# Kernel tuning notes

Hardware: AMD Instinct MI355X
Metric: run time of the kernel (lower is better)

Reference implementation:

```python
import jax, jax.numpy as jnp
import numpy as np
from jax import lax

L, H, NUM_CONVS, KSIZE = 8192, 128, 4, 7
EPS = 1e-5


def _pos_encoding(length, dim, dtype):
    pos = jnp.arange(length, dtype=jnp.float32)[:, None]
    i = jnp.arange(dim, dtype=jnp.float32)[None, :]
    angle = pos / jnp.power(10000.0, (2.0 * jnp.floor(i / 2.0)) / dim)
    pe = jnp.where((jnp.arange(dim) % 2 == 0)[None, :], jnp.sin(angle), jnp.cos(angle))
    return pe.astype(dtype)


def _layer_norm(x):
    mu = jnp.mean(x, axis=-1, keepdims=True)
    var = jnp.mean(jnp.square(x - mu), axis=-1, keepdims=True)
    return (x - mu) * lax.rsqrt(var + EPS)


def _conv1d_same(x, w, b):
    # x: [L, H]; w: [H_out, H_in, K]; b: [H_out]. SAME padding over sequence.
    lhs = x.T[None]  # [1, H, L]
    out = lax.conv_general_dilated(lhs, w, window_strides=(1,), padding='SAME',
                                   dimension_numbers=('NCH', 'OIH', 'NCH'))
    return (out[0] + b[:, None]).T  # [L, H]


def setup_inputs() -> dict:
    key = jax.random.key(0)
    ks = jax.random.split(key, 12)
    s = 0.02
    return {
        'x': jax.random.normal(ks[0], (L, H), jnp.float32),
        'conv_w': jax.random.normal(ks[1], (NUM_CONVS, H, H, KSIZE), jnp.float32) * s,
        'conv_b': jax.random.normal(ks[2], (NUM_CONVS, H), jnp.float32) * s,
        'Wq': jax.random.normal(ks[3], (H, H), jnp.float32) * s,
        'bq': jax.random.normal(ks[4], (H,), jnp.float32) * s,
        'Wk': jax.random.normal(ks[5], (H, H), jnp.float32) * s,
        'bk': jax.random.normal(ks[6], (H,), jnp.float32) * s,
        'Wv': jax.random.normal(ks[7], (H, H), jnp.float32) * s,
        'bv': jax.random.normal(ks[8], (H,), jnp.float32) * s,
        'Wff': jax.random.normal(ks[9], (H, H), jnp.float32) * s,
        'bff': jax.random.normal(ks[10], (H,), jnp.float32) * s,
    }


def reference(x, conv_w, conv_b, Wq, bq, Wk, bk, Wv, bv, Wff, bff):
    h = x + _pos_encoding(x.shape[0], x.shape[1], x.dtype)
    # conv stack: LN -> conv -> residual, repeated num_convs times
    for i in range(NUM_CONVS):
        residual = h
        h = _conv1d_same(_layer_norm(h), conv_w[i], conv_b[i]) + residual
    # self-attention (single-head as written in the source)
    residual = h
    n = _layer_norm(h)
    q = n @ Wq.T + bq
    k = n @ Wk.T + bk
    v = n @ Wv.T + bv
    scale = 1.0 / jnp.sqrt(jnp.asarray(H, h.dtype))
    attn = jax.nn.softmax((q @ k.T) * scale, axis=-1)  # [L, L]
    h = attn @ v + residual
    # feed-forward
    residual = h
    h = jax.nn.relu(_layer_norm(h) @ Wff.T + bff) + residual
    return h
```

## Files before the change

kernel.cpp:

```cpp
#include <hip/hip_runtime.h>

#define LL 8192
#define HH 128

typedef __attribute__((ext_vector_type(8))) short short8v;
typedef __attribute__((ext_vector_type(4))) short short4v;
typedef __attribute__((ext_vector_type(4))) float f32x4;

__device__ inline short f2bf(float f) {
    union { float f; unsigned u; } x; x.f = f;
    unsigned r = (x.u + 0x7fffu + ((x.u >> 16) & 1u)) >> 16;
    return (short)r;
}
__device__ inline float bf2f(short s) {
    union { unsigned u; float f; } x; x.u = ((unsigned)(unsigned short)s) << 16;
    return x.f;
}

__device__ inline short* sAp(short* base, int row, int col) {
    int byte = (row << 8) + (col << 1);
    byte ^= (row & 7) << 4;
    return (short*)((char*)base + byte);
}

__device__ inline short8v ln_pack8(const float* rowF, int l15) {
    const float4 a = *(const float4*)&rowF[l15 * 8];
    const float4 b = *(const float4*)&rowF[l15 * 8 + 4];
    float s  = (a.x + a.y) + (a.z + a.w) + (b.x + b.y) + (b.z + b.w);
    float s2 = a.x * a.x + a.y * a.y + a.z * a.z + a.w * a.w
             + b.x * b.x + b.y * b.y + b.z * b.z + b.w * b.w;
#pragma unroll
    for (int off = 1; off <= 8; off <<= 1) {
        s  += __shfl_xor(s,  off, 64);
        s2 += __shfl_xor(s2, off, 64);
    }
    float mu = s * (1.f / 128.f);
    float var = s2 * (1.f / 128.f) - mu * mu;
    float rstd = rsqrtf(var + 1e-5f);
    short8v r;
    r[0] = f2bf((a.x - mu) * rstd);
    r[1] = f2bf((a.y - mu) * rstd);
    r[2] = f2bf((a.z - mu) * rstd);
    r[3] = f2bf((a.w - mu) * rstd);
    r[4] = f2bf((b.x - mu) * rstd);
    r[5] = f2bf((b.y - mu) * rstd);
    r[6] = f2bf((b.z - mu) * rstd);
    r[7] = f2bf((b.w - mu) * rstd);
    return r;
}

__global__ __launch_bounds__(256) void repack_all(const float* __restrict__ x,
                                                  const float* __restrict__ w,
                                                  const float* __restrict__ Wq,
                                                  const float* __restrict__ Wk,
                                                  const float* __restrict__ Wv,
                                                  const float* __restrict__ bq,
                                                  const float* __restrict__ bk,
                                                  const float* __restrict__ bv,
                                                  const float* __restrict__ Wff,
                                                  short* __restrict__ wkb,
                                                  short* __restrict__ wqkvb,
                                                  float* __restrict__ b3,
                                                  short* __restrict__ wffb,
                                                  float* __restrict__ h0) {
    const float qs = 0.08838834764831845f;
    int idx = blockIdx.x * 256 + threadIdx.x;
    if (idx < 458752) {
        int k = idx % 7;
        int t = idx / 7;
        int i = t % HH; t /= HH;
        int o = t % HH;
        int lay = t / HH;
        wkb[((lay * 7 + k) * HH + o) * HH + i] = f2bf(w[idx]);
    } else {
        int j = idx - 458752;
        if (j < 49152) {
            int t = j >> 14, r = j & 16383;
            float v = (t == 0) ? Wq[r] * qs : (t == 1) ? Wk[r] : Wv[r];
            wqkvb[j] = f2bf(v);
        } else if (j < 49536) {
            int jj = j - 49152;
            b3[jj] = (jj < 128) ? bq[jj] * qs : (jj < 256) ? bk[jj - 128] : bv[jj - 256];
        } else if (j < 65920) {
            int jj = j - 49536;
            wffb[jj] = f2bf(Wff[jj]);
        } else {
            int p = j - 65920;
            if (p < 262144) {
                int g = p >> 5, c4 = (p & 31) << 2;
                float4 val = *(const float4*)&x[g * HH + c4];
                float fg = (float)g;
#pragma unroll
                for (int h = 0; h < 2; h++) {
                    int i0 = c4 + h * 2;
                    float e = (float)i0 / 128.f;
                    float ang = fg / powf(10000.f, e);
                    ((float*)&val)[h * 2]     += sinf(ang);
                    ((float*)&val)[h * 2 + 1] += cosf(ang);
                }
                *(float4*)&h0[g * HH + c4] = val;
            }
        }
    }
}

__global__ __launch_bounds__(256, 4) void conv_layer_kernel(const float* __restrict__ hin,
                                                            const short* __restrict__ wkb,
                                                            const float* __restrict__ conv_b,
                                                            float* __restrict__ hout,
                                                            int lay) {
    __shared__ float sF[22][132];
    __shared__ short sA[22 * 128];
    int tid = threadIdx.x;
    int w = tid >> 6, lane = tid & 63;
    int l15 = lane & 15, quad = lane >> 4;
    int m0 = (blockIdx.x >> 1) * 16;
    int c0w = (blockIdx.x & 1) * 64 + w * 16;

    for (int idx = tid; idx < 22 * 32; idx += 256) {
        int r = idx >> 5, c4 = (idx & 31) << 2;
        int g = m0 - 3 + r;
        float4 val = make_float4(0.f, 0.f, 0.f, 0.f);
        if (g >= 0 && g < LL) val = *(const float4*)&hin[g * HH + c4];
        *(float4*)&sF[r][c4] = val;
    }
    __syncthreads();
#pragma unroll
    for (int rr = 0; rr < 2; rr++) {
        int row = rr * 16 + w * 4 + quad;
        if (row < 22)
            *(short8v*)sAp(sA, row, l15 * 8) = ln_pack8(&sF[row][0], l15);
    }
    __syncthreads();
    f32x4 accA = (f32x4)(0.f), accB = (f32x4)(0.f);
    const short* wl = wkb + lay * 7 * HH * HH;
    for (int k = 0; k < 7; k++) {
        const short* b0 = wl + (k * HH + c0w + l15) * HH;
#pragma unroll
        for (int ks = 0; ks < 4; ks++) {
            short8v bf = *(const short8v*)&b0[ks * 32 + quad * 8];
            short8v af = *(const short8v*)sAp(sA, l15 + k, ks * 32 + quad * 8);
            if (ks & 1) accB = __builtin_amdgcn_mfma_f32_16x16x32_bf16(af, bf, accB, 0, 0, 0);
            else        accA = __builtin_amdgcn_mfma_f32_16x16x32_bf16(af, bf, accA, 0, 0, 0);
        }
    }
    float bb = conv_b[lay * HH + c0w + l15];
#pragma unroll
    for (int r = 0; r < 4; r++) {
        int row = quad * 4 + r;
        hout[(m0 + row) * HH + c0w + l15] =
            sF[3 + row][c0w + l15] + accA[r] + accB[r] + bb;
    }
}

__global__ __launch_bounds__(256, 4) void qkv_kernel(const float* __restrict__ h4,
                                                     const short* __restrict__ wqkvb,
                                                     const float* __restrict__ b3,
                                                     short* __restrict__ qb,
                                                     short* __restrict__ kb,
                                                     short* __restrict__ vt) {
    __shared__ float sF[16][132];
    __shared__ short sA[16 * 128];
    __shared__ short sT[4][32][17];
    int tid = threadIdx.x;
    int w = tid >> 6, lane = tid & 63;
    int l15 = lane & 15, quad = lane >> 4;
    int m0 = blockIdx.x * 16;
    int t = blockIdx.y;

    for (int idx = tid; idx < 16 * 32; idx += 256) {
        int r = idx >> 5, c4 = (idx & 31) << 2;
        *(float4*)&sF[r][c4] = *(const float4*)&h4[(m0 + r) * HH + c4];
    }
    __syncthreads();
    {
        int row = w * 4 + quad;
        *(short8v*)sAp(sA, row, l15 * 8) = ln_pack8(&sF[row][0], l15);
    }
    __syncthreads();
    int c0 = w * 32;
    f32x4 acc0 = (f32x4)(0.f), acc1 = (f32x4)(0.f);
    const short* b0 = wqkvb + (t * 128 + c0 + l15) * HH;
    const short* b1 = b0 + 16 * HH;
#pragma unroll
    for (int ks = 0; ks < 4; ks++) {
        short8v af = *(const short8v*)sAp(sA, l15, ks * 32 + quad * 8);
        short8v bf0 = *(const short8v*)&b0[ks * 32 + quad * 8];
        short8v bf1 = *(const short8v*)&b1[ks * 32 + quad * 8];
        acc0 = __builtin_amdgcn_mfma_f32_16x16x32_bf16(af, bf0, acc0, 0, 0, 0);
        acc1 = __builtin_amdgcn_mfma_f32_16x16x32_bf16(af, bf1, acc1, 0, 0, 0);
    }
    float bb0 = b3[t * 128 + c0 + l15], bb1 = b3[t * 128 + c0 + 16 + l15];
    if (t < 2) {
        short* o = (t == 0) ? qb : kb;
#pragma unroll
        for (int r = 0; r < 4; r++) {
            int lr = m0 + quad * 4 + r;
            o[lr * HH + c0 + l15]      = f2bf(acc0[r] + bb0);
            o[lr * HH + c0 + 16 + l15] = f2bf(acc1[r] + bb1);
        }
    } else {
#pragma unroll
        for (int r = 0; r < 4; r++) {
            sT[w][l15][quad * 4 + r]      = f2bf(acc0[r] + bb0);
            sT[w][16 + l15][quad * 4 + r] = f2bf(acc1[r] + bb1);
        }
        asm volatile("s_waitcnt lgkmcnt(0)" ::: "memory");
#pragma unroll
        for (int cc = 0; cc < 8; cc++) {
            int col = cc * 4 + quad;
            vt[(c0 + col) * LL + m0 + l15] = sT[w][col][l15];
        }
    }
}

#define FBN 64

__global__ __launch_bounds__(256, 2) void flash_mfma_kernel(const short* __restrict__ qs,
                                                            const short* __restrict__ ksrc,
                                                            const short* __restrict__ vsrc,
                                                            short* __restrict__ PO,
                                                            float* __restrict__ Pl,
                                                            int segrows) {
    __shared__ short sK[16 * 64 * 8];
    __shared__ short sV[16 * 64 * 8];
    __shared__ short sP[4][32][72];

    const int tid = threadIdx.x;
    const int w = tid >> 6, lane = tid & 63;
    const int l15 = lane & 15, quad = lane >> 4;
    const int m0 = blockIdx.x * 128;
    const int seg = blockIdx.y;
    const int jbeg = seg * segrows;
    const int nchunk = segrows >> 6;

    const int vdt_base = (w >> 1);
    const int vks2 = w & 1;

    short8v qf[2][4];
#pragma unroll
    for (int mt = 0; mt < 2; mt++)
#pragma unroll
        for (int ks = 0; ks < 4; ks++)
            qf[mt][ks] = *(const short8v*)&qs[(m0 + w * 32 + mt * 16 + l15) * HH + ks * 32 + quad * 8];

    float l_r[2][4] = {{0.f, 0.f, 0.f, 0.f}, {0.f, 0.f, 0.f, 0.f}};
    f32x4 o_acc[2][8];
#pragma unroll
    for (int mt = 0; mt < 2; mt++)
#pragma unroll
        for (int dt = 0; dt < 8; dt++) o_acc[mt][dt] = (f32x4)(0.f);

    short8v kr[4], vr[4];
#pragma unroll
    for (int r = 0; r < 4; r++) {
        kr[r] = *(const short8v*)&ksrc[(jbeg + r * 16 + l15) * HH + w * 32 + quad * 8];
        vr[r] = *(const short8v*)&vsrc[((2 * r + vdt_base) * 16 + l15) * LL + jbeg + vks2 * 32 + quad * 8];
    }

    for (int c = 0; c < nchunk; c++) {
        __syncthreads();
#pragma unroll
        for (int r = 0; r < 4; r++) {
            *(short8v*)&sK[((w + 4 * r) * 64 + lane) * 8] = kr[r];
            *(short8v*)&sV[((w + 4 * r) * 64 + lane) * 8] = vr[r];
        }
        __syncthreads();
        if (c + 1 < nchunk) {
            const int j1 = jbeg + (c + 1) * FBN;
#pragma unroll
            for (int r = 0; r < 4; r++) {
                kr[r] = *(const short8v*)&ksrc[(j1 + r * 16 + l15) * HH + w * 32 + quad * 8];
                vr[r] = *(const short8v*)&vsrc[((2 * r + vdt_base) * 16 + l15) * LL + j1 + vks2 * 32 + quad * 8];
            }
        }
        f32x4 s_acc[2][4];
#pragma unroll
        for (int mt = 0; mt < 2; mt++)
#pragma unroll
            for (int nt = 0; nt < 4; nt++) s_acc[mt][nt] = (f32x4)(0.f);
#pragma unroll
        for (int nt = 0; nt < 4; nt++)
#pragma unroll
            for (int ks = 0; ks < 4; ks++) {
                short8v kf = *(const short8v*)&sK[((nt * 4 + ks) * 64 + lane) * 8];
                s_acc[0][nt] = __builtin_amdgcn_mfma_f32_16x16x32_bf16(qf[0][ks], kf, s_acc[0][nt], 0, 0, 0);
                s_acc[1][nt] = __builtin_amdgcn_mfma_f32_16x16x32_bf16(qf[1][ks], kf, s_acc[1][nt], 0, 0, 0);
            }
#pragma unroll
        for (int mt = 0; mt < 2; mt++)
#pragma unroll
            for (int nt = 0; nt < 4; nt++)
#pragma unroll
                for (int r = 0; r < 4; r++) {
                    float p = __expf(fminf(s_acc[mt][nt][r], 30.f));
                    l_r[mt][r] += p;
                    union { float f; unsigned u; } cv; cv.f = p;
                    sP[w][mt * 16 + quad * 4 + r][nt * 16 + l15] = (short)(cv.u >> 16);
                }
        asm volatile("s_waitcnt lgkmcnt(0)" ::: "memory");
#pragma unroll
        for (int ks2 = 0; ks2 < 2; ks2++) {
            short8v pf0 = *(const short8v*)&sP[w][l15][ks2 * 32 + quad * 8];
            short8v pf1 = *(const short8v*)&sP[w][16 + l15][ks2 * 32 + quad * 8];
#pragma unroll
            for (int dt = 0; dt < 8; dt++) {
                short8v vf = *(const short8v*)&sV[((dt * 2 + ks2) * 64 + lane) * 8];
                o_acc[0][dt] = __builtin_amdgcn_mfma_f32_16x16x32_bf16(pf0, vf, o_acc[0][dt], 0, 0, 0);
                o_acc[1][dt] = __builtin_amdgcn_mfma_f32_16x16x32_bf16(pf1, vf, o_acc[1][dt], 0, 0, 0);
            }
        }
    }
#pragma unroll
    for (int mt = 0; mt < 2; mt++)
#pragma unroll
        for (int r = 0; r < 4; r++) {
            float v = l_r[mt][r];
            v += __shfl_xor(v, 1, 64);
            v += __shfl_xor(v, 2, 64);
            v += __shfl_xor(v, 4, 64);
            v += __shfl_xor(v, 8, 64);
            if (l15 == 0)
                Pl[seg * LL + m0 + w * 32 + mt * 16 + quad * 4 + r] = v;
        }
#pragma unroll
    for (int mt = 0; mt < 2; mt++)
#pragma unroll
        for (int dt = 0; dt < 8; dt++)
#pragma unroll
            for (int r = 0; r < 4; r++)
                PO[(size_t)seg * LL * HH + (m0 + w * 32 + mt * 16 + quad * 4 + r) * HH + dt * 16 + l15] =
                    f2bf(o_acc[mt][dt][r]);
}

__global__ __launch_bounds__(256) void ff_kernel(const float* __restrict__ hin,
                                                 const short* __restrict__ PO,
                                                 const float* __restrict__ Pl,
                                                 const short* __restrict__ wffb,
                                                 const float* __restrict__ bff,
                                                 float* __restrict__ out,
                                                 int nsplit) {
    __shared__ float sF[16][132];
    __shared__ short sA[16 * 128];
    __shared__ float sLi[16];
    int tid = threadIdx.x;
    int w = tid >> 6, lane = tid & 63;
    int l15 = lane & 15, quad = lane >> 4;
    int m0 = blockIdx.x * 16;

    if (tid < 16) {
        float s = 0.f;
        for (int seg = 0; seg < nsplit; seg++) s += Pl[seg * LL + m0 + tid];
        sLi[tid] = 1.f / s;
    }
    __syncthreads();
    for (int idx = tid; idx < 16 * 32; idx += 256) {
        int r = idx >> 5, c4 = (idx & 31) << 2;
        float4 hv = *(const float4*)&hin[(m0 + r) * HH + c4];
        float s0 = 0.f, s1 = 0.f, s2 = 0.f, s3 = 0.f;
        for (int seg = 0; seg < nsplit; seg++) {
            short4v pv = *(const short4v*)&PO[(size_t)seg * LL * HH + (m0 + r) * HH + c4];
            s0 += bf2f(pv[0]); s1 += bf2f(pv[1]); s2 += bf2f(pv[2]); s3 += bf2f(pv[3]);
        }
        float li = sLi[r];
        *(float4*)&sF[r][c4] = make_float4(hv.x + s0 * li, hv.y + s1 * li,
                                           hv.z + s2 * li, hv.w + s3 * li);
    }
    __syncthreads();
    {
        int row = w * 4 + quad;
        *(short8v*)sAp(sA, row, l15 * 8) = ln_pack8(&sF[row][0], l15);
    }
    __syncthreads();
    int c0 = w * 32;
    f32x4 acc0 = (f32x4)(0.f), acc1 = (f32x4)(0.f);
    const short* b0 = wffb + (c0 + l15) * HH;
    const short* b1 = b0 + 16 * HH;
#pragma unroll
    for (int ks = 0; ks < 4; ks++) {
        short8v af = *(const short8v*)sAp(sA, l15, ks * 32 + quad * 8);
        short8v bf0 = *(const short8v*)&b0[ks * 32 + quad * 8];
        short8v bf1 = *(const short8v*)&b1[ks * 32 + quad * 8];
        acc0 = __builtin_amdgcn_mfma_f32_16x16x32_bf16(af, bf0, acc0, 0, 0, 0);
        acc1 = __builtin_amdgcn_mfma_f32_16x16x32_bf16(af, bf1, acc1, 0, 0, 0);
    }
    float bb0 = bff[c0 + l15], bb1 = bff[c0 + 16 + l15];
#pragma unroll
    for (int r = 0; r < 4; r++) {
        int lr = quad * 4 + r;
        out[(m0 + lr) * HH + c0 + l15]      = fmaxf(acc0[r] + bb0, 0.f) + sF[lr][c0 + l15];
        out[(m0 + lr) * HH + c0 + 16 + l15] = fmaxf(acc1[r] + bb1, 0.f) + sF[lr][c0 + 16 + l15];
    }
}

extern "C" void kernel_launch(void* const* d_in, const int* in_sizes, int n_in,
                              void* d_out, int out_size, void* d_ws, size_t ws_size,
                              hipStream_t stream) {
    const float* x      = (const float*)d_in[0];
    const float* conv_w = (const float*)d_in[1];
    const float* conv_b = (const float*)d_in[2];
    const float* Wq = (const float*)d_in[3];
    const float* bq = (const float*)d_in[4];
    const float* Wk = (const float*)d_in[5];
    const float* bk = (const float*)d_in[6];
    const float* Wv = (const float*)d_in[7];
    const float* bv = (const float*)d_in[8];
    const float* Wff = (const float*)d_in[9];
    const float* bff = (const float*)d_in[10];
    float* out = (float*)d_out;

    char* ws = (char*)d_ws;
    const size_t MB = 1u << 20;
    float* hB   = (float*)(ws);
    short* qb   = (short*)(ws + 4 * MB);
    short* kb   = (short*)(ws + 6 * MB);
    short* vt   = (short*)(ws + 8 * MB);
    float* Pl   = (float*)(ws + 10 * MB);
    short* wffb = (short*)(ws + 10 * MB + 524288);
    short* PO   = (short*)(ws + 10 * MB + 524288 + 32768);
    short* wkb   = (short*)(ws + 16 * MB);
    short* wqkvb = (short*)(ws + 17 * MB);
    float* b3    = (float*)(ws + 17 * MB + 131072);
    float* h0    = (float*)(ws + 18 * MB);
    float* h13   = (float*)(ws + 22 * MB);
    float* h2    = h0;

    int nsplit = (ws_size >= (size_t)44 * MB) ? 16 : 8;
    int segrows = LL / nsplit;

    repack_all<<<3074, 256, 0, stream>>>(x, conv_w, Wq, Wk, Wv, bq, bk, bv, Wff,
                                         wkb, wqkvb, b3, wffb, h0);
    conv_layer_kernel<<<LL / 16 * 2, 256, 0, stream>>>(h0,  wkb, conv_b, h13, 0);
    conv_layer_kernel<<<LL / 16 * 2, 256, 0, stream>>>(h13, wkb, conv_b, h2,  1);
    conv_layer_kernel<<<LL / 16 * 2, 256, 0, stream>>>(h2,  wkb, conv_b, h13, 2);
    conv_layer_kernel<<<LL / 16 * 2, 256, 0, stream>>>(h13, wkb, conv_b, hB,  3);
    qkv_kernel<<<dim3(LL / 16, 3), 256, 0, stream>>>(hB, wqkvb, b3, qb, kb, vt);
    flash_mfma_kernel<<<dim3(LL / 128, nsplit), 256, 0, stream>>>(qb, kb, vt, PO, Pl, segrows);
    ff_kernel<<<LL / 16, 256, 0, stream>>>(hB, PO, Pl, wffb, bff, out, nsplit);
}
```

Baseline: 229.6 us.

## Switch flash attention to 32x32x16 MFMA and keep P in registers

Rewrites the flash attention inner loop to use 32x32x16 bf16 MFMA tiles. S is computed transposed (K as the A operand) so the exponentiated P values can be packed to bf16 and rearranged with v_permlane32_swap into the A-operand layout for the PV MFMA. This removes the shared-memory round trip through sP along with its wait. It also fixes the split count at 8 instead of choosing 16 when workspace allows, which changes grid parallelism and the partial-reduction work in ff_kernel.

```diff
diff --git a/kernel.cpp b/kernel.cpp
--- a/kernel.cpp
+++ b/kernel.cpp
@@ -6,6 +6,7 @@
 typedef __attribute__((ext_vector_type(8))) short short8v;
 typedef __attribute__((ext_vector_type(4))) short short4v;
 typedef __attribute__((ext_vector_type(4))) float f32x4;
+typedef __attribute__((ext_vector_type(16))) float f32x16;
 
 __device__ inline short f2bf(float f) {
     union { float f; unsigned u; } x; x.f = f;
@@ -15,6 +16,18 @@
 __device__ inline float bf2f(short s) {
     union { unsigned u; float f; } x; x.u = ((unsigned)(unsigned short)s) << 16;
     return x.f;
+}
+
+__device__ inline void plane32swap(unsigned& a, unsigned& b) {
+#if defined(__has_builtin)
+#if __has_builtin(__builtin_amdgcn_permlane32_swap)
+    typedef unsigned u2v __attribute__((ext_vector_type(2)));
+    u2v r = __builtin_amdgcn_permlane32_swap(a, b, false, false);
+    a = r[0]; b = r[1];
+    return;
+#endif
+#endif
+    asm volatile("v_permlane32_swap_b32 %0, %1" : "+v"(a), "+v"(b));
 }
 
 __device__ inline short* sAp(short* base, int row, int col) {
@@ -224,113 +237,103 @@
                                                             int segrows) {
     __shared__ short sK[16 * 64 * 8];
     __shared__ short sV[16 * 64 * 8];
-    __shared__ short sP[4][32][72];
 
     const int tid = threadIdx.x;
     const int w = tid >> 6, lane = tid & 63;
-    const int l15 = lane & 15, quad = lane >> 4;
+    const int l31 = lane & 31, hi = lane >> 5;
     const int m0 = blockIdx.x * 128;
     const int seg = blockIdx.y;
     const int jbeg = seg * segrows;
     const int nchunk = segrows >> 6;
-
-    const int vdt_base = (w >> 1);
-    const int vks2 = w & 1;
-
-    short8v qf[2][4];
-#pragma unroll
-    for (int mt = 0; mt < 2; mt++)
-#pragma unroll
-        for (int ks = 0; ks < 4; ks++)
-            qf[mt][ks] = *(const short8v*)&qs[(m0 + w * 32 + mt * 16 + l15) * HH + ks * 32 + quad * 8];
-
-    float l_r[2][4] = {{0.f, 0.f, 0.f, 0.f}, {0.f, 0.f, 0.f, 0.f}};
-    f32x4 o_acc[2][8];
-#pragma unroll
-    for (int mt = 0; mt < 2; mt++)
-#pragma unroll
-        for (int dt = 0; dt < 8; dt++) o_acc[mt][dt] = (f32x4)(0.f);
+    const int qrow = m0 + w * 32 + l31;
+
+    short8v qf[8];
+#pragma unroll
+    for (int ks = 0; ks < 8; ks++)
+        qf[ks] = *(const short8v*)&qs[qrow * HH + ks * 16 + hi * 8];
+
+    float l_r = 0.f;
+    f32x16 o_acc[4];
+#pragma unroll
+    for (int dt = 0; dt < 4; dt++) o_acc[dt] = (f32x16)(0.f);
 
     short8v kr[4], vr[4];
 #pragma unroll
     for (int r = 0; r < 4; r++) {
-        kr[r] = *(const short8v*)&ksrc[(jbeg + r * 16 + l15) * HH + w * 32 + quad * 8];
-        vr[r] = *(const short8v*)&vsrc[((2 * r + vdt_base) * 16 + l15) * LL + jbeg + vks2 * 32 + quad * 8];
+        int s = w + 4 * r;
+        kr[r] = *(const short8v*)&ksrc[(jbeg + (s >> 3) * 32 + l31) * HH + (s & 7) * 16 + hi * 8];
+        vr[r] = *(const short8v*)&vsrc[((s >> 2) * 32 + l31) * LL + jbeg + (s & 3) * 16 + hi * 8];
     }
 
     for (int c = 0; c < nchunk; c++) {
         __syncthreads();
 #pragma unroll
         for (int r = 0; r < 4; r++) {
-            *(short8v*)&sK[((w + 4 * r) * 64 + lane) * 8] = kr[r];
-            *(short8v*)&sV[((w + 4 * r) * 64 + lane) * 8] = vr[r];
+            int s = w + 4 * r;
+            *(short8v*)&sK[(s * 64 + lane) * 8] = kr[r];
+            *(short8v*)&sV[(s * 64 + lane) * 8] = vr[r];
         }
         __syncthreads();
         if (c + 1 < nchunk) {
             const int j1 = jbeg + (c + 1) * FBN;
 #pragma unroll
             for (int r = 0; r < 4; r++) {
-                kr[r] = *(const short8v*)&ksrc[(j1 + r * 16 + l15) * HH + w * 32 + quad * 8];
-                vr[r] = *(const short8v*)&vsrc[((2 * r + vdt_base) * 16 + l15) * LL + j1 + vks2 * 32 + quad * 8];
+                int s = w + 4 * r;
+                kr[r] = *(const short8v*)&ksrc[(j1 + (s >> 3) * 32 + l31) * HH + (s & 7) * 16 + hi * 8];
+                vr[r] = *(const short8v*)&vsrc[((s >> 2) * 32 + l31) * LL + j1 + (s & 3) * 16 + hi * 8];
             }
         }
-        f32x4 s_acc[2][4];
-#pragma unroll
-        for (int mt = 0; mt < 2; mt++)
-#pragma unroll
-            for (int nt = 0; nt < 4; nt++) s_acc[mt][nt] = (f32x4)(0.f);
-#pragma unroll
-        for (int nt = 0; nt < 4; nt++)
-#pragma unroll
-            for (int ks = 0; ks < 4; ks++) {
-                short8v kf = *(const short8v*)&sK[((nt * 4 + ks) * 64 + lane) * 8];
-                s_acc[0][nt] = __builtin_amdgcn_mfma_f32_16x16x32_bf16(qf[0][ks], kf, s_acc[0][nt], 0, 0, 0);
-                s_acc[1][nt] = __builtin_amdgcn_mfma_f32_16x16x32_bf16(qf[1][ks], kf, s_acc[1][nt], 0, 0, 0);
+        f32x16 s0 = (f32x16)(0.f), s1 = (f32x16)(0.f);
+#pragma unroll
+        for (int ks = 0; ks < 8; ks++) {
+            short8v kf0 = *(const short8v*)&sK[((ks) * 64 + lane) * 8];
+            short8v kf1 = *(const short8v*)&sK[((8 + ks) * 64 + lane) * 8];
+            s0 = __builtin_amdgcn_mfma_f32_32x32x16_bf16(kf0, qf[ks], s0, 0, 0, 0);
+            s1 = __builtin_amdgcn_mfma_f32_32x32x16_bf16(kf1, qf[ks], s1, 0, 0, 0);
+        }
+        short8v pfrag[4];
+#pragma unroll
+        for (int nt = 0; nt < 2; nt++) {
+            const f32x16& sa = nt ? s1 : s0;
+            unsigned pw[8];
+#pragma unroll
+            for (int m = 0; m < 8; m++) {
+                float p0 = __expf(fminf(sa[2 * m], 30.f));
+                float p1 = __expf(fminf(sa[2 * m + 1], 30.f));
+                l_r += p0 + p1;
+                union { float f; unsigned u; } u0, u1;
+                u0.f = p0; u1.f = p1;
+                pw[m] = (u0.u >> 16) | (u1.u & 0xffff0000u);
             }
-#pragma unroll
-        for (int mt = 0; mt < 2; mt++)
-#pragma unroll
-            for (int nt = 0; nt < 4; nt++)
-#pragma unroll
-                for (int r = 0; r < 4; r++) {
-                    float p = __expf(fminf(s_acc[mt][nt][r], 30.f));
-                    l_r[mt][r] += p;
-                    union { float f; unsigned u; } cv; cv.f = p;
-                    sP[w][mt * 16 + quad * 4 + r][nt * 16 + l15] = (short)(cv.u >> 16);
-                }
-        asm volatile("s_waitcnt lgkmcnt(0)" ::: "memory");
-#pragma unroll
-        for (int ks2 = 0; ks2 < 2; ks2++) {
-            short8v pf0 = *(const short8v*)&sP[w][l15][ks2 * 32 + quad * 8];
-            short8v pf1 = *(const short8v*)&sP[w][16 + l15][ks2 * 32 + quad * 8];
-#pragma unroll
-            for (int dt = 0; dt < 8; dt++) {
-                short8v vf = *(const short8v*)&sV[((dt * 2 + ks2) * 64 + lane) * 8];
-                o_acc[0][dt] = __builtin_amdgcn_mfma_f32_16x16x32_bf16(pf0, vf, o_acc[0][dt], 0, 0, 0);
-                o_acc[1][dt] = __builtin_amdgcn_mfma_f32_16x16x32_bf16(pf1, vf, o_acc[1][dt], 0, 0, 0);
+            plane32swap(pw[0], pw[2]);
+            plane32swap(pw[1], pw[3]);
+            plane32swap(pw[4], pw[6]);
+            plane32swap(pw[5], pw[7]);
+            union { unsigned u[4]; short8v v; } fa, fb;
+            fa.u[0] = pw[0]; fa.u[1] = pw[1]; fa.u[2] = pw[2]; fa.u[3] = pw[3];
+            fb.u[0] = pw[4]; fb.u[1] = pw[5]; fb.u[2] = pw[6]; fb.u[3] = pw[7];
+            pfrag[nt * 2]     = fa.v;
+            pfrag[nt * 2 + 1] = fb.v;
+        }
+#pragma unroll
+        for (int ks = 0; ks < 4; ks++)
+#pragma unroll
+            for (int dt = 0; dt < 4; dt++) {
+                short8v vf = *(const short8v*)&sV[((dt * 4 + ks) * 64 + lane) * 8];
+                o_acc[dt] = __builtin_amdgcn_mfma_f32_32x32x16_bf16(pfrag[ks], vf, o_acc[dt], 0, 0, 0);
             }
-        }
-    }
-#pragma unroll
-    for (int mt = 0; mt < 2; mt++)
-#pragma unroll
-        for (int r = 0; r < 4; r++) {
-            float v = l_r[mt][r];
-            v += __shfl_xor(v, 1, 64);
-            v += __shfl_xor(v, 2, 64);
-            v += __shfl_xor(v, 4, 64);
-            v += __shfl_xor(v, 8, 64);
-            if (l15 == 0)
-                Pl[seg * LL + m0 + w * 32 + mt * 16 + quad * 4 + r] = v;
-        }
-#pragma unroll
-    for (int mt = 0; mt < 2; mt++)
-#pragma unroll
-        for (int dt = 0; dt < 8; dt++)
-#pragma unroll
-            for (int r = 0; r < 4; r++)
-                PO[(size_t)seg * LL * HH + (m0 + w * 32 + mt * 16 + quad * 4 + r) * HH + dt * 16 + l15] =
-                    f2bf(o_acc[mt][dt][r]);
+    }
+    float lsum = l_r + __shfl_xor(l_r, 32, 64);
+    if (hi == 0)
+        Pl[seg * LL + qrow] = lsum;
+#pragma unroll
+    for (int dt = 0; dt < 4; dt++)
+#pragma unroll
+        for (int i = 0; i < 16; i++) {
+            int qr = (i & 3) + 8 * (i >> 2) + 4 * hi;
+            PO[(size_t)seg * LL * HH + (size_t)(m0 + w * 32 + qr) * HH + dt * 32 + l31] =
+                f2bf(o_acc[dt][i]);
+        }
 }
 
 __global__ __launch_bounds__(256) void ff_kernel(const float* __restrict__ hin,
@@ -425,8 +428,8 @@
     float* h13   = (float*)(ws + 22 * MB);
     float* h2    = h0;
 
-    int nsplit = (ws_size >= (size_t)44 * MB) ? 16 : 8;
-    int segrows = LL / nsplit;
+    const int nsplit = 8;
+    const int segrows = LL / nsplit;
 
     repack_all<<<3074, 256, 0, stream>>>(x, conv_w, Wq, Wk, Wv, bq, bk, bv, Wff,
                                          wkb, wqkvb, b3, wffb, h0);
```

After: 214.7 us. 6.5% less time.
